# Performance work log

Hardware: AMD Instinct MI355X
Metric: run time of the kernel (lower is better)

The kernel has to match this reference:

```python
import jax, jax.numpy as jnp
import numpy as np

D_MODEL = 256
N_HEADS = 8
HEAD_DIM = D_MODEL // N_HEADS


def setup_inputs() -> dict:
    key = jax.random.key(0)
    k1, k2, k3, k4, k5, k6, k7 = jax.random.split(key, 7)
    B, T, N, D = 4, 32, 32, D_MODEL
    x = jax.random.normal(k1, (B, T, N, D), dtype=jnp.float32)
    bias_features = jax.random.normal(k2, (B, T, N, N, D), dtype=jnp.float32)
    # alive mask, mostly True so rows are rarely fully masked
    mask = jax.random.uniform(k3, (B, T, N)) < 0.9
    s = 1.0 / np.sqrt(D)
    w_qkv = jax.random.normal(k4, (D, 3 * D), dtype=jnp.float32) * s
    b_qkv = jnp.zeros((3 * D,), dtype=jnp.float32)
    w_proj = jax.random.normal(k5, (D, D), dtype=jnp.float32) * s
    b_proj = jnp.zeros((D,), dtype=jnp.float32)
    return {"x": x, "bias_features": bias_features, "mask": mask,
            "w_qkv": w_qkv, "b_qkv": b_qkv, "w_proj": w_proj, "b_proj": b_proj}


def reference(x, bias_features, mask, w_qkv, b_qkv, w_proj, b_proj):
    B, T, N, D = x.shape
    H, Dh = N_HEADS, D // N_HEADS
    Bt = B * T
    xf = x.reshape(Bt, N, D)
    qkv = xf @ w_qkv + b_qkv                       # (Bt, N, 3D)
    q, k, v = jnp.split(qkv, 3, axis=-1)
    q = q.reshape(Bt, N, H, Dh)
    k = k.reshape(Bt, N, H, Dh)
    v = v.reshape(Bt, N, H, Dh)
    b_geo = bias_features.reshape(Bt, N, N, H, Dh)
    k_pair = k[:, None] + b_geo                    # (Bt, N, N, H, Dh)
    v_pair = v[:, None] + b_geo
    # scores: (Bt, H, N, N)
    scores = jnp.einsum('bihd,bijhd->bhij', q, k_pair) * (Dh ** -0.5)
    mask_flat = mask.reshape(Bt, 1, 1, N)
    scores = jnp.where(mask_flat, scores, -jnp.inf)
    max_scores = jnp.max(scores, axis=-1, keepdims=True)
    is_nan_row = max_scores == -jnp.inf
    scores_safe = jnp.where(is_nan_row, 0.0, scores)
    attn = jax.nn.softmax(scores_safe, axis=-1)
    attn = jnp.where(is_nan_row, 0.0, attn)
    out = jnp.einsum('bhij,bijhd->bihd', attn, v_pair).reshape(Bt, N, D)
    out = out.reshape(B, T, N, D)
    return out @ w_proj + b_proj
```

## Files before the change

### kernel.cpp

```cpp
#include <hip/hip_runtime.h>
#include <math.h>

typedef __attribute__((ext_vector_type(8))) short bf16x8;
typedef __attribute__((ext_vector_type(4))) float f32x4;

__device__ inline ushort f2bf(float f) {
    union { float f; uint u; } v; v.f = f;
    uint u = v.u;
    uint r = (u + 0x7fff + ((u >> 16) & 1)) >> 16;
    return (ushort)r;
}

__global__ __launch_bounds__(256) void prep_kernel(
    const float* __restrict__ x, const float* __restrict__ wqkv,
    const float* __restrict__ wproj,
    ushort* __restrict__ xb, ushort* __restrict__ wqkvT, ushort* __restrict__ wprojT)
{
    const int b = blockIdx.x, t = threadIdx.x;
    if (b < 512) {
        size_t i8 = (size_t)(b * 256 + t);
        const float4* src = (const float4*)x + i8 * 2;
        float4 v0 = src[0], v1 = src[1];
        bf16x8 o;
        o[0] = (short)f2bf(v0.x); o[1] = (short)f2bf(v0.y);
        o[2] = (short)f2bf(v0.z); o[3] = (short)f2bf(v0.w);
        o[4] = (short)f2bf(v1.x); o[5] = (short)f2bf(v1.y);
        o[6] = (short)f2bf(v1.z); o[7] = (short)f2bf(v1.w);
        *(bf16x8*)(xb + i8 * 8) = o;
    } else if (b < 704) {
        int q = (b - 512) * 256 + t;
        int n4 = q % 192, k = q / 192;
        float4 v = *(const float4*)&wqkv[(size_t)k * 768 + n4 * 4];
        wqkvT[(size_t)(n4 * 4 + 0) * 256 + k] = f2bf(v.x);
        wqkvT[(size_t)(n4 * 4 + 1) * 256 + k] = f2bf(v.y);
        wqkvT[(size_t)(n4 * 4 + 2) * 256 + k] = f2bf(v.z);
        wqkvT[(size_t)(n4 * 4 + 3) * 256 + k] = f2bf(v.w);
    } else {
        int q = (b - 704) * 256 + t;
        int n4 = q % 64, k = q / 64;
        float4 v = *(const float4*)&wproj[(size_t)k * 256 + n4 * 4];
        wprojT[(size_t)(n4 * 4 + 0) * 256 + k] = f2bf(v.x);
        wprojT[(size_t)(n4 * 4 + 1) * 256 + k] = f2bf(v.y);
        wprojT[(size_t)(n4 * 4 + 2) * 256 + k] = f2bf(v.z);
        wprojT[(size_t)(n4 * 4 + 3) * 256 + k] = f2bf(v.w);
    }
}

template<int BM, int BN, int WGM, int WGN>
__global__ __launch_bounds__(WGM * WGN * 64) void mfma_gemm_bt(
    const ushort* __restrict__ A, const ushort* __restrict__ BT,
    const float* __restrict__ bias, float* __restrict__ C,
    int M, int N, int K)
{
    constexpr int BK = 32;
    constexpr int NT = WGM * WGN * 64;
    constexpr int WM = BM / (WGM * 16);
    constexpr int WN = BN / (WGN * 16);

    __shared__ ushort As[BM * BK];
    __shared__ ushort Bs[BN * BK];

    const int tid = threadIdx.x;
    const int lane = tid & 63, wid = tid >> 6;
    const int wm = wid / WGN, wn = wid % WGN;
    const int row0 = blockIdx.x * BM, col0 = blockIdx.y * BN;
    const int frow = lane & 15, fg = lane >> 4;

    f32x4 acc[WM][WN] = {};

    for (int k0 = 0; k0 < K; k0 += BK) {
        #pragma unroll
        for (int ci = tid; ci < BM * 4; ci += NT) {
            int r = ci >> 2, g = ci & 3;
            bf16x8 v = *(const bf16x8*)&A[(size_t)(row0 + r) * K + k0 + g * 8];
            *(bf16x8*)&As[r * 32 + ((g ^ ((r >> 1) & 3)) << 3)] = v;
        }
        #pragma unroll
        for (int ci = tid; ci < BN * 4; ci += NT) {
            int r = ci >> 2, g = ci & 3;
            bf16x8 v = *(const bf16x8*)&BT[(size_t)(col0 + r) * K + k0 + g * 8];
            *(bf16x8*)&Bs[r * 32 + ((g ^ ((r >> 1) & 3)) << 3)] = v;
        }
        __syncthreads();

        bf16x8 af[WM], bf[WN];
        #pragma unroll
        for (int m = 0; m < WM; ++m) {
            int r = (wm * WM + m) * 16 + frow;
            af[m] = *(const bf16x8*)&As[r * 32 + ((fg ^ ((r >> 1) & 3)) << 3)];
        }
        #pragma unroll
        for (int n = 0; n < WN; ++n) {
            int r = (wn * WN + n) * 16 + frow;
            bf[n] = *(const bf16x8*)&Bs[r * 32 + ((fg ^ ((r >> 1) & 3)) << 3)];
        }
        #pragma unroll
        for (int m = 0; m < WM; ++m)
            #pragma unroll
            for (int n = 0; n < WN; ++n)
                acc[m][n] = __builtin_amdgcn_mfma_f32_16x16x32_bf16(
                    af[m], bf[n], acc[m][n], 0, 0, 0);
        __syncthreads();
    }

    #pragma unroll
    for (int n = 0; n < WN; ++n) {
        int gcol = col0 + (wn * WN + n) * 16 + (lane & 15);
        float bv = bias[gcol];
        #pragma unroll
        for (int m = 0; m < WM; ++m) {
            int grow0 = row0 + (wm * WM + m) * 16 + (lane >> 4) * 4;
            #pragma unroll
            for (int r = 0; r < 4; ++r)
                C[(size_t)(grow0 + r) * N + gcol] = acc[m][n][r] + bv;
        }
    }
}

__global__ __launch_bounds__(256) void relattn_kernel(
    const float* __restrict__ qkv, const float* __restrict__ bias,
    const int* __restrict__ mask, ushort* __restrict__ attn_out)
{
    __shared__ float bias_lds[8192];
    __shared__ float p_lds[256];

    const int blk = blockIdx.x;
    const int bt = blk >> 5;
    const int tid = threadIdx.x;

    const float* bsrc = bias + (size_t)blk * 8192;
    #pragma unroll
    for (int it = 0; it < 8; ++it) {
        int idx4 = it * 256 + tid;
        float4 v = *(const float4*)(bsrc + (size_t)idx4 * 4);
        int j = idx4 >> 6, c = idx4 & 63;
        int dst4 = (j << 6) | (c ^ (j & 7));
        *(float4*)&bias_lds[dst4 * 4] = v;
    }
    __syncthreads();

    const int j = tid & 31, h = tid >> 5;
    const float* qrow = qkv + (size_t)blk * 768 + h * 32;
    const float* krow = qkv + (size_t)(bt * 32 + j) * 768 + 256 + h * 32;
    float s = 0.f;
    #pragma unroll
    for (int d4 = 0; d4 < 8; ++d4) {
        float4 qv = *(const float4*)(qrow + d4 * 4);
        float4 kv = *(const float4*)(krow + d4 * 4);
        int c = (h * 8 + d4) ^ (j & 7);
        float4 bv = *(const float4*)&bias_lds[(j * 64 + c) * 4];
        s += qv.x * (kv.x + bv.x) + qv.y * (kv.y + bv.y)
           + qv.z * (kv.z + bv.z) + qv.w * (kv.w + bv.w);
    }
    s *= 0.17677669529663687f;

    const bool alive = (mask[bt * 32 + j] != 0);
    s = alive ? s : -__builtin_inff();

    float m = s;
    #pragma unroll
    for (int off = 16; off; off >>= 1) m = fmaxf(m, __shfl_xor(m, off));
    const bool dead = (m == -__builtin_inff());
    float p = alive ? __expf(s - m) : 0.f;
    float l = p;
    #pragma unroll
    for (int off = 16; off; off >>= 1) l += __shfl_xor(l, off);
    float pn = dead ? 0.f : p / l;
    p_lds[tid] = pn;
    __syncthreads();

    const float* vcol = qkv + (size_t)bt * 32 * 768 + 512 + tid;
    const int hbase = tid & 0xE0;
    float o = 0.f;
    #pragma unroll
    for (int jj = 0; jj < 32; ++jj) {
        float pv = p_lds[hbase + jj];
        float vv = vcol[(size_t)jj * 768];
        int cblk = (tid >> 2) ^ (jj & 7);
        float bb = bias_lds[(jj * 64 + cblk) * 4 + (tid & 3)];
        o += pv * (vv + bb);
    }
    attn_out[(size_t)blk * 256 + tid] = f2bf(o);
}

extern "C" void kernel_launch(void* const* d_in, const int* in_sizes, int n_in,
                              void* d_out, int out_size, void* d_ws, size_t ws_size,
                              hipStream_t stream) {
    const float* x      = (const float*)d_in[0];
    const float* bias_f = (const float*)d_in[1];
    const int*   mask   = (const int*)d_in[2];
    const float* w_qkv  = (const float*)d_in[3];
    const float* b_qkv  = (const float*)d_in[4];
    const float* w_proj = (const float*)d_in[5];
    const float* b_proj = (const float*)d_in[6];
    float* out = (float*)d_out;

    char* ws = (char*)d_ws;
    float*  qkv      = (float*)ws;
    ushort* xb       = (ushort*)(ws + 12582912);
    ushort* attn_o   = xb;
    ushort* wqkvT    = (ushort*)(ws + 14680064);
    ushort* wprojT   = (ushort*)(ws + 15073280);

    prep_kernel<<<768, 256, 0, stream>>>(x, w_qkv, w_proj, xb, wqkvT, wprojT);

    mfma_gemm_bt<128, 64, 2, 2><<<dim3(4096 / 128, 768 / 64), 256, 0, stream>>>(
        xb, wqkvT, b_qkv, qkv, 4096, 768, 256);

    relattn_kernel<<<4096, 256, 0, stream>>>(qkv, bias_f, mask, attn_o);

    mfma_gemm_bt<64, 64, 2, 2><<<dim3(4096 / 64, 256 / 64), 256, 0, stream>>>(
        attn_o, wprojT, b_proj, out, 4096, 256, 256);
}
```

Baseline: 67.74 us.

## Fuse bf16 conversion into GEMMs, store QKV as bf16, async bias load

Removes the separate prep kernel by converting x and the fp32 weights to bf16 inside the GEMM tile loads, transposing the weights on the fly. The QKV GEMM now writes separate bf16 q/k/v buffers instead of fp32 qkv, halving the attention kernel's q/k/v read traffic. The bias tile is loaded into LDS with global_load_lds when that builtin exists, and the GEMM tile shapes change. In exchange the weights are re-converted by every block, the B-tile LDS writes become scalar 2-byte stores, and q/k/v lose precision to bf16.

```diff
diff --git a/kernel.cpp b/kernel.cpp
--- a/kernel.cpp
+++ b/kernel.cpp
@@ -2,55 +2,38 @@
 #include <math.h>
 
 typedef __attribute__((ext_vector_type(8))) short bf16x8;
+typedef __attribute__((ext_vector_type(4))) short bf16x4;
 typedef __attribute__((ext_vector_type(4))) float f32x4;
 
 __device__ inline ushort f2bf(float f) {
     union { float f; uint u; } v; v.f = f;
     uint u = v.u;
-    uint r = (u + 0x7fff + ((u >> 16) & 1)) >> 16;
-    return (ushort)r;
-}
-
-__global__ __launch_bounds__(256) void prep_kernel(
-    const float* __restrict__ x, const float* __restrict__ wqkv,
-    const float* __restrict__ wproj,
-    ushort* __restrict__ xb, ushort* __restrict__ wqkvT, ushort* __restrict__ wprojT)
-{
-    const int b = blockIdx.x, t = threadIdx.x;
-    if (b < 512) {
-        size_t i8 = (size_t)(b * 256 + t);
-        const float4* src = (const float4*)x + i8 * 2;
-        float4 v0 = src[0], v1 = src[1];
-        bf16x8 o;
-        o[0] = (short)f2bf(v0.x); o[1] = (short)f2bf(v0.y);
-        o[2] = (short)f2bf(v0.z); o[3] = (short)f2bf(v0.w);
-        o[4] = (short)f2bf(v1.x); o[5] = (short)f2bf(v1.y);
-        o[6] = (short)f2bf(v1.z); o[7] = (short)f2bf(v1.w);
-        *(bf16x8*)(xb + i8 * 8) = o;
-    } else if (b < 704) {
-        int q = (b - 512) * 256 + t;
-        int n4 = q % 192, k = q / 192;
-        float4 v = *(const float4*)&wqkv[(size_t)k * 768 + n4 * 4];
-        wqkvT[(size_t)(n4 * 4 + 0) * 256 + k] = f2bf(v.x);
-        wqkvT[(size_t)(n4 * 4 + 1) * 256 + k] = f2bf(v.y);
-        wqkvT[(size_t)(n4 * 4 + 2) * 256 + k] = f2bf(v.z);
-        wqkvT[(size_t)(n4 * 4 + 3) * 256 + k] = f2bf(v.w);
-    } else {
-        int q = (b - 704) * 256 + t;
-        int n4 = q % 64, k = q / 64;
-        float4 v = *(const float4*)&wproj[(size_t)k * 256 + n4 * 4];
-        wprojT[(size_t)(n4 * 4 + 0) * 256 + k] = f2bf(v.x);
-        wprojT[(size_t)(n4 * 4 + 1) * 256 + k] = f2bf(v.y);
-        wprojT[(size_t)(n4 * 4 + 2) * 256 + k] = f2bf(v.z);
-        wprojT[(size_t)(n4 * 4 + 3) * 256 + k] = f2bf(v.w);
-    }
-}
-
-template<int BM, int BN, int WGM, int WGN>
-__global__ __launch_bounds__(WGM * WGN * 64) void mfma_gemm_bt(
-    const ushort* __restrict__ A, const ushort* __restrict__ BT,
-    const float* __restrict__ bias, float* __restrict__ C,
-    int M, int N, int K)
+    return (ushort)((u + 0x7fff + ((u >> 16) & 1)) >> 16);
+}
+__device__ inline float bf2f(ushort u) {
+    union { uint u; float f; } v; v.u = ((uint)u) << 16; return v.f;
+}
+
+#ifndef __has_builtin
+#define __has_builtin(x) 0
+#endif
+#if __has_builtin(__builtin_amdgcn_global_load_lds)
+#define HAVE_GLL 1
+typedef __attribute__((address_space(1))) const void global_void;
+typedef __attribute__((address_space(3))) void lds_void;
+__device__ inline void gl_lds16(const void* g, void* l) {
+    __builtin_amdgcn_global_load_lds((global_void*)g, (lds_void*)l, 16, 0, 0);
+}
+#else
+#define HAVE_GLL 0
+#endif
+
+template<int BM, int BN, int WGM, int WGN, int MODE>
+__global__ __launch_bounds__(WGM * WGN * 64) void gemm_fused(
+    const void* __restrict__ Ap, const float* __restrict__ Bw, int ldb,
+    const float* __restrict__ bias,
+    void* __restrict__ C0, void* __restrict__ C1, void* __restrict__ C2,
+    int K, int N)
 {
     constexpr int BK = 32;
     constexpr int NT = WGM * WGN * 64;
@@ -63,27 +46,44 @@
     const int tid = threadIdx.x;
     const int lane = tid & 63, wid = tid >> 6;
     const int wm = wid / WGN, wn = wid % WGN;
-    const int row0 = blockIdx.x * BM, col0 = blockIdx.y * BN;
+    const int row0 = blockIdx.y * BM, col0 = blockIdx.x * BN;
     const int frow = lane & 15, fg = lane >> 4;
 
     f32x4 acc[WM][WN] = {};
 
     for (int k0 = 0; k0 < K; k0 += BK) {
-        #pragma unroll
-        for (int ci = tid; ci < BM * 4; ci += NT) {
-            int r = ci >> 2, g = ci & 3;
-            bf16x8 v = *(const bf16x8*)&A[(size_t)(row0 + r) * K + k0 + g * 8];
-            *(bf16x8*)&As[r * 32 + ((g ^ ((r >> 1) & 3)) << 3)] = v;
-        }
-        #pragma unroll
-        for (int ci = tid; ci < BN * 4; ci += NT) {
-            int r = ci >> 2, g = ci & 3;
-            bf16x8 v = *(const bf16x8*)&BT[(size_t)(col0 + r) * K + k0 + g * 8];
-            *(bf16x8*)&Bs[r * 32 + ((g ^ ((r >> 1) & 3)) << 3)] = v;
+        if constexpr (MODE == 0) {
+            #pragma unroll
+            for (int ci = tid; ci < BM * 8; ci += NT) {
+                int r = ci >> 3, kq = ci & 7, g = kq >> 1;
+                float4 v = *(const float4*)((const float*)Ap + (size_t)(row0 + r) * K + k0 + kq * 4);
+                bf16x4 o;
+                o[0] = (short)f2bf(v.x); o[1] = (short)f2bf(v.y);
+                o[2] = (short)f2bf(v.z); o[3] = (short)f2bf(v.w);
+                *(bf16x4*)&As[r * 32 + ((g ^ ((r >> 1) & 3)) << 3) + (kq & 1) * 4] = o;
+            }
+        } else {
+            #pragma unroll
+            for (int ci = tid; ci < BM * 4; ci += NT) {
+                int r = ci >> 2, g = ci & 3;
+                bf16x8 v = *(const bf16x8*)((const ushort*)Ap + (size_t)(row0 + r) * K + k0 + g * 8);
+                *(bf16x8*)&As[r * 32 + ((g ^ ((r >> 1) & 3)) << 3)] = v;
+            }
+        }
+        #pragma unroll
+        for (int ci = tid; ci < BN * 8; ci += NT) {
+            int kk = ci & 31, n4 = ci >> 5;
+            float4 v = *(const float4*)&Bw[(size_t)(k0 + kk) * ldb + col0 + n4 * 4];
+            float vv[4] = {v.x, v.y, v.z, v.w};
+            #pragma unroll
+            for (int e = 0; e < 4; ++e) {
+                int n = n4 * 4 + e;
+                Bs[n * 32 + (((kk >> 3) ^ ((n >> 1) & 3)) << 3) + (kk & 7)] = f2bf(vv[e]);
+            }
         }
         __syncthreads();
 
-        bf16x8 af[WM], bf[WN];
+        bf16x8 af[WM], bfr[WN];
         #pragma unroll
         for (int m = 0; m < WM; ++m) {
             int r = (wm * WM + m) * 16 + frow;
@@ -92,33 +92,47 @@
         #pragma unroll
         for (int n = 0; n < WN; ++n) {
             int r = (wn * WN + n) * 16 + frow;
-            bf[n] = *(const bf16x8*)&Bs[r * 32 + ((fg ^ ((r >> 1) & 3)) << 3)];
+            bfr[n] = *(const bf16x8*)&Bs[r * 32 + ((fg ^ ((r >> 1) & 3)) << 3)];
         }
         #pragma unroll
         for (int m = 0; m < WM; ++m)
             #pragma unroll
             for (int n = 0; n < WN; ++n)
                 acc[m][n] = __builtin_amdgcn_mfma_f32_16x16x32_bf16(
-                    af[m], bf[n], acc[m][n], 0, 0, 0);
+                    af[m], bfr[n], acc[m][n], 0, 0, 0);
         __syncthreads();
     }
 
     #pragma unroll
     for (int n = 0; n < WN; ++n) {
-        int gcol = col0 + (wn * WN + n) * 16 + (lane & 15);
+        int gcol = col0 + (wn * WN + n) * 16 + frow;
         float bv = bias[gcol];
-        #pragma unroll
-        for (int m = 0; m < WM; ++m) {
-            int grow0 = row0 + (wm * WM + m) * 16 + (lane >> 4) * 4;
-            #pragma unroll
-            for (int r = 0; r < 4; ++r)
-                C[(size_t)(grow0 + r) * N + gcol] = acc[m][n][r] + bv;
+        if constexpr (MODE == 0) {
+            int b = gcol >> 8, c = gcol & 255;
+            ushort* dst = (b == 0) ? (ushort*)C0 : (b == 1) ? (ushort*)C1 : (ushort*)C2;
+            #pragma unroll
+            for (int m = 0; m < WM; ++m) {
+                int grow0 = row0 + (wm * WM + m) * 16 + fg * 4;
+                #pragma unroll
+                for (int r = 0; r < 4; ++r)
+                    dst[(size_t)(grow0 + r) * 256 + c] = f2bf(acc[m][n][r] + bv);
+            }
+        } else {
+            float* dst = (float*)C0;
+            #pragma unroll
+            for (int m = 0; m < WM; ++m) {
+                int grow0 = row0 + (wm * WM + m) * 16 + fg * 4;
+                #pragma unroll
+                for (int r = 0; r < 4; ++r)
+                    dst[(size_t)(grow0 + r) * N + gcol] = acc[m][n][r] + bv;
+            }
         }
     }
 }
 
 __global__ __launch_bounds__(256) void relattn_kernel(
-    const float* __restrict__ qkv, const float* __restrict__ bias,
+    const ushort* __restrict__ qb, const ushort* __restrict__ kb,
+    const ushort* __restrict__ vb, const float* __restrict__ bias,
     const int* __restrict__ mask, ushort* __restrict__ attn_out)
 {
     __shared__ float bias_lds[8192];
@@ -127,30 +141,46 @@
     const int blk = blockIdx.x;
     const int bt = blk >> 5;
     const int tid = threadIdx.x;
-
+    const int lane = tid & 63, wid = tid >> 6;
     const float* bsrc = bias + (size_t)blk * 8192;
+
+#if HAVE_GLL
+    #pragma unroll
+    for (int it = 0; it < 8; ++it) {
+        int j = it * 4 + wid;
+        const float* src = bsrc + (size_t)((j << 6) | (lane ^ (j & 7))) * 4;
+        gl_lds16(src, &bias_lds[j * 256]);
+    }
+#else
     #pragma unroll
     for (int it = 0; it < 8; ++it) {
         int idx4 = it * 256 + tid;
         float4 v = *(const float4*)(bsrc + (size_t)idx4 * 4);
         int j = idx4 >> 6, c = idx4 & 63;
-        int dst4 = (j << 6) | (c ^ (j & 7));
-        *(float4*)&bias_lds[dst4 * 4] = v;
-    }
+        *(float4*)&bias_lds[((j << 6) | (c ^ (j & 7))) * 4] = v;
+    }
+#endif
     __syncthreads();
 
     const int j = tid & 31, h = tid >> 5;
-    const float* qrow = qkv + (size_t)blk * 768 + h * 32;
-    const float* krow = qkv + (size_t)(bt * 32 + j) * 768 + 256 + h * 32;
+    const ushort* qrow = qb + (size_t)blk * 256 + h * 32;
+    const ushort* krow = kb + (size_t)(bt * 32 + j) * 256 + h * 32;
     float s = 0.f;
     #pragma unroll
-    for (int d4 = 0; d4 < 8; ++d4) {
-        float4 qv = *(const float4*)(qrow + d4 * 4);
-        float4 kv = *(const float4*)(krow + d4 * 4);
-        int c = (h * 8 + d4) ^ (j & 7);
-        float4 bv = *(const float4*)&bias_lds[(j * 64 + c) * 4];
-        s += qv.x * (kv.x + bv.x) + qv.y * (kv.y + bv.y)
-           + qv.z * (kv.z + bv.z) + qv.w * (kv.w + bv.w);
+    for (int it = 0; it < 4; ++it) {
+        bf16x8 q8 = *(const bf16x8*)(qrow + it * 8);
+        bf16x8 k8 = *(const bf16x8*)(krow + it * 8);
+        int c0 = h * 8 + it * 2;
+        float4 b0 = *(const float4*)&bias_lds[((j << 6) | (c0 ^ (j & 7))) * 4];
+        float4 b1 = *(const float4*)&bias_lds[((j << 6) | ((c0 + 1) ^ (j & 7))) * 4];
+        s += bf2f((ushort)q8[0]) * (bf2f((ushort)k8[0]) + b0.x)
+           + bf2f((ushort)q8[1]) * (bf2f((ushort)k8[1]) + b0.y)
+           + bf2f((ushort)q8[2]) * (bf2f((ushort)k8[2]) + b0.z)
+           + bf2f((ushort)q8[3]) * (bf2f((ushort)k8[3]) + b0.w)
+           + bf2f((ushort)q8[4]) * (bf2f((ushort)k8[4]) + b1.x)
+           + bf2f((ushort)q8[5]) * (bf2f((ushort)k8[5]) + b1.y)
+           + bf2f((ushort)q8[6]) * (bf2f((ushort)k8[6]) + b1.z)
+           + bf2f((ushort)q8[7]) * (bf2f((ushort)k8[7]) + b1.w);
     }
     s *= 0.17677669529663687f;
 
@@ -165,17 +195,16 @@
     float l = p;
     #pragma unroll
     for (int off = 16; off; off >>= 1) l += __shfl_xor(l, off);
-    float pn = dead ? 0.f : p / l;
-    p_lds[tid] = pn;
+    p_lds[tid] = dead ? 0.f : p / l;
     __syncthreads();
 
-    const float* vcol = qkv + (size_t)bt * 32 * 768 + 512 + tid;
+    const ushort* vcol = vb + (size_t)bt * 32 * 256 + tid;
     const int hbase = tid & 0xE0;
     float o = 0.f;
     #pragma unroll
     for (int jj = 0; jj < 32; ++jj) {
         float pv = p_lds[hbase + jj];
-        float vv = vcol[(size_t)jj * 768];
+        float vv = bf2f(vcol[(size_t)jj * 256]);
         int cblk = (tid >> 2) ^ (jj & 7);
         float bb = bias_lds[(jj * 64 + cblk) * 4 + (tid & 3)];
         o += pv * (vv + bb);
@@ -195,20 +224,16 @@
     const float* b_proj = (const float*)d_in[6];
     float* out = (float*)d_out;
 
-    char* ws = (char*)d_ws;
-    float*  qkv      = (float*)ws;
-    ushort* xb       = (ushort*)(ws + 12582912);
-    ushort* attn_o   = xb;
-    ushort* wqkvT    = (ushort*)(ws + 14680064);
-    ushort* wprojT   = (ushort*)(ws + 15073280);
-
-    prep_kernel<<<768, 256, 0, stream>>>(x, w_qkv, w_proj, xb, wqkvT, wprojT);
-
-    mfma_gemm_bt<128, 64, 2, 2><<<dim3(4096 / 128, 768 / 64), 256, 0, stream>>>(
-        xb, wqkvT, b_qkv, qkv, 4096, 768, 256);
-
-    relattn_kernel<<<4096, 256, 0, stream>>>(qkv, bias_f, mask, attn_o);
-
-    mfma_gemm_bt<64, 64, 2, 2><<<dim3(4096 / 64, 256 / 64), 256, 0, stream>>>(
-        attn_o, wprojT, b_proj, out, 4096, 256, 256);
-}
+    ushort* qb = (ushort*)d_ws;
+    ushort* kb = qb + (size_t)4096 * 256;
+    ushort* vb = kb + (size_t)4096 * 256;
+    ushort* ao = vb + (size_t)4096 * 256;
+
+    gemm_fused<64, 64, 2, 2, 0><<<dim3(12, 64), 256, 0, stream>>>(
+        x, w_qkv, 768, b_qkv, qb, kb, vb, 256, 768);
+
+    relattn_kernel<<<4096, 256, 0, stream>>>(qb, kb, vb, bias_f, mask, ao);
+
+    gemm_fused<32, 64, 1, 4, 1><<<dim3(4, 128), 256, 0, stream>>>(
+        ao, w_proj, 256, b_proj, out, nullptr, nullptr, 256, 256);
+}
```

Measured after the change: 60.42 us. 1.12x faster.
